# Kernel tuning notes

Hardware: AMD Instinct MI355X
Metric: run time of the kernel (lower is better)

## Reference

```python
import jax, jax.numpy as jnp
import numpy as np

TAU = 2.0      # LIF membrane time constant
ALPHA = 4.0    # spikingjelly surrogate.Sigmoid default alpha
V_TH = 1.0     # LIF threshold
EPS = 1e-5     # BatchNorm eps
NUM_HEADS = 8
TOPK = 64      # int(0.25 * 256)


@jax.custom_vjp
def spike_fn(x):
    # Heaviside spike with sigmoid surrogate gradient
    return (x >= 0.0).astype(x.dtype)

def _spike_fwd(x):
    return spike_fn(x), x

def _spike_bwd(x, g):
    s = jax.nn.sigmoid(ALPHA * x)
    return (g * ALPHA * s * (1.0 - s),)

spike_fn.defvjp(_spike_fwd, _spike_bwd)


def lif(x_seq):
    # Multi-step LIF (decay_input=True, hard reset to 0, detach_reset=True).
    # x_seq: [T, ...]; returns spikes of same shape.
    def step(v, x):
        v = v + (x - v) / TAU
        s = spike_fn(v - V_TH)
        v = v * (1.0 - jax.lax.stop_gradient(s))
        return v, s
    _, spikes = jax.lax.scan(step, jnp.zeros_like(x_seq[0]), x_seq)
    return spikes


def bn_eval(x, p):
    # BatchNorm in eval mode over last axis; p rows = [gamma, beta, mean, var]
    gamma, beta, mean, var = p[0], p[1], p[2], p[3]
    return (x - mean) * (gamma * jax.lax.rsqrt(var + EPS)) + beta


def setup_inputs() -> dict:
    key = jax.random.key(0)
    ks = jax.random.split(key, 10)
    T, B, N, C, H = 4, 16, 256, 256, NUM_HEADS
    w_scale = C ** -0.5
    return {
        "x": jax.random.normal(ks[0], (T, B, N, C), jnp.float32),
        "wq": jax.random.normal(ks[1], (C, C), jnp.float32) * w_scale,
        "wk": jax.random.normal(ks[2], (C, C), jnp.float32) * w_scale,
        "wv": jax.random.normal(ks[3], (C, C), jnp.float32) * w_scale,
        "bnq": jax.random.uniform(ks[4], (4, C), jnp.float32, 0.1, 1.0),
        "bnk": jax.random.uniform(ks[5], (4, C), jnp.float32, 0.1, 1.0),
        "bnv": jax.random.uniform(ks[6], (4, C), jnp.float32, 0.1, 1.0),
        "proj_w": jax.random.normal(ks[7], (C, C), jnp.float32) * w_scale,
        "proj_bn": jax.random.uniform(ks[8], (4, C), jnp.float32, 0.1, 1.0),
        "rel_bias_table": jax.random.normal(ks[9], (2 * N - 1, H), jnp.float32),
    }


def reference(x, wq, wk, wv, bnq, bnk, bnv, proj_w, proj_bn, rel_bias_table):
    T, B, N, C = x.shape
    H = NUM_HEADS
    D = C // H
    scale = C ** -0.5

    def qkv_branch(w, bn_p):
        h = jnp.einsum('tbnc,oc->tbno', x, w)   # Linear (no bias)
        h = bn_eval(h, bn_p)                    # eval BN is per-channel affine
        s = lif(h)                              # [T,B,N,C] spikes
        return s.reshape(T, B, N, H, D).transpose(0, 1, 3, 2, 4)  # [T,B,H,N,D]

    q = qkv_branch(wq, bnq)
    k = qkv_branch(wk, bnk)
    v = qkv_branch(wv, bnv)

    attn = jnp.einsum('tbhnd,tbhmd->tbhnm', q, k) * scale  # [T,B,H,N,N]

    # relative position bias gather: table[(j - i) + (N-1)] -> [N,N,H]
    rel_idx = (jnp.arange(N)[None, :] - jnp.arange(N)[:, None]) + (N - 1)
    rel_bias = rel_bias_table[rel_idx]                      # [N,N,H]
    attn = attn + rel_bias.transpose(2, 0, 1)[None, None]   # bcast over T,B

    # top-k keep per row, others zeroed (no softmax)
    kth = jax.lax.stop_gradient(jax.lax.top_k(attn, TOPK)[0][..., -1:])
    attn = jnp.where(attn >= kth, attn, 0.0)

    out = jnp.einsum('tbhnm,tbhmd->tbhnd', attn, v)
    out = out.transpose(0, 1, 3, 2, 4).reshape(T, B, N, C)
    out = lif(out)  # attn_lif

    # proj SpikLinearLayer: Linear -> BN(eval) -> LIF
    h = jnp.einsum('tbnc,oc->tbno', out, proj_w)
    h = bn_eval(h, proj_bn)
    return lif(h)
```

## Files before the change

### kernel.cpp

```cpp
#include <hip/hip_runtime.h>

typedef unsigned int u32;
typedef unsigned long long u64;

#define T_ 4
#define B_ 16
#define N_ 256
#define C_ 256
#define H_ 8
#define D_ 32
#define BNC_ 1048576
#define NELEM 4194304

__global__ __launch_bounds__(256) void gemm_bn(
    const float* __restrict__ A, const float* __restrict__ W,
    const float* __restrict__ bnp, float* __restrict__ Out)
{
  __shared__ float As[32][68];
  __shared__ float Ws[32][68];
  const int tid = threadIdx.x;
  const int m0 = blockIdx.y << 6;
  const int n0 = blockIdx.x << 6;
  const int tx = tid & 15, ty = tid >> 4;
  const int lrow = tid >> 3;
  const int lk = (tid & 7) << 2;

  float acc[4][4] = {};

  for (int k0 = 0; k0 < 256; k0 += 32) {
    float4 a0 = *(const float4*)(A + (size_t)(m0 + lrow) * 256 + k0 + lk);
    float4 a1 = *(const float4*)(A + (size_t)(m0 + lrow + 32) * 256 + k0 + lk);
    float4 w0 = *(const float4*)(W + (size_t)(n0 + lrow) * 256 + k0 + lk);
    float4 w1 = *(const float4*)(W + (size_t)(n0 + lrow + 32) * 256 + k0 + lk);
    __syncthreads();
    As[lk+0][lrow] = a0.x; As[lk+1][lrow] = a0.y; As[lk+2][lrow] = a0.z; As[lk+3][lrow] = a0.w;
    As[lk+0][lrow+32] = a1.x; As[lk+1][lrow+32] = a1.y; As[lk+2][lrow+32] = a1.z; As[lk+3][lrow+32] = a1.w;
    Ws[lk+0][lrow] = w0.x; Ws[lk+1][lrow] = w0.y; Ws[lk+2][lrow] = w0.z; Ws[lk+3][lrow] = w0.w;
    Ws[lk+0][lrow+32] = w1.x; Ws[lk+1][lrow+32] = w1.y; Ws[lk+2][lrow+32] = w1.z; Ws[lk+3][lrow+32] = w1.w;
    __syncthreads();
#pragma unroll
    for (int kk = 0; kk < 32; ++kk) {
      float4 av = *(const float4*)&As[kk][ty << 2];
      float4 bv = *(const float4*)&Ws[kk][tx << 2];
      acc[0][0] = fmaf(av.x, bv.x, acc[0][0]);
      acc[0][1] = fmaf(av.x, bv.y, acc[0][1]);
      acc[0][2] = fmaf(av.x, bv.z, acc[0][2]);
      acc[0][3] = fmaf(av.x, bv.w, acc[0][3]);
      acc[1][0] = fmaf(av.y, bv.x, acc[1][0]);
      acc[1][1] = fmaf(av.y, bv.y, acc[1][1]);
      acc[1][2] = fmaf(av.y, bv.z, acc[1][2]);
      acc[1][3] = fmaf(av.y, bv.w, acc[1][3]);
      acc[2][0] = fmaf(av.z, bv.x, acc[2][0]);
      acc[2][1] = fmaf(av.z, bv.y, acc[2][1]);
      acc[2][2] = fmaf(av.z, bv.z, acc[2][2]);
      acc[2][3] = fmaf(av.z, bv.w, acc[2][3]);
      acc[3][0] = fmaf(av.w, bv.x, acc[3][0]);
      acc[3][1] = fmaf(av.w, bv.y, acc[3][1]);
      acc[3][2] = fmaf(av.w, bv.z, acc[3][2]);
      acc[3][3] = fmaf(av.w, bv.w, acc[3][3]);
    }
  }

  const float* gma = bnp;
  const float* bta = bnp + 256;
  const float* mea = bnp + 512;
  const float* vra = bnp + 768;
  float sc[4], me[4], be[4];
#pragma unroll
  for (int jj = 0; jj < 4; ++jj) {
    int o = n0 + (tx << 2) + jj;
    sc[jj] = __fmul_rn(gma[o], 1.0f / sqrtf(__fadd_rn(vra[o], 1e-5f)));
    me[jj] = mea[o];
    be[jj] = bta[o];
  }
#pragma unroll
  for (int ii = 0; ii < 4; ++ii) {
    int row = m0 + (ty << 2) + ii;
    float4 y;
    y.x = __fadd_rn(__fmul_rn(__fsub_rn(acc[ii][0], me[0]), sc[0]), be[0]);
    y.y = __fadd_rn(__fmul_rn(__fsub_rn(acc[ii][1], me[1]), sc[1]), be[1]);
    y.z = __fadd_rn(__fmul_rn(__fsub_rn(acc[ii][2], me[2]), sc[2]), be[2]);
    y.w = __fadd_rn(__fmul_rn(__fsub_rn(acc[ii][3], me[3]), sc[3]), be[3]);
    *(float4*)(Out + (size_t)row * 256 + n0 + (tx << 2)) = y;
  }
}

__global__ __launch_bounds__(256) void lif_pack3(
    const float* __restrict__ h0, const float* __restrict__ h1,
    const float* __restrict__ h2,
    u32* __restrict__ m0p, u32* __restrict__ m1p, u32* __restrict__ m2p)
{
  const float* h = (blockIdx.y == 0) ? h0 : (blockIdx.y == 1) ? h1 : h2;
  u32* mask      = (blockIdx.y == 0) ? m0p : (blockIdx.y == 1) ? m1p : m2p;
  const int blk = blockIdx.x;
  const int b = blk >> 8, n = blk & 255;
  const int c = threadIdx.x;
  const int wave = c >> 6, lane = c & 63;
  const size_t idx = ((size_t)b * 256 + n) * 256 + c;
  float v = 0.0f;
#pragma unroll
  for (int t = 0; t < 4; ++t) {
    float xv = h[idx + (size_t)t * BNC_];
    v = __fadd_rn(v, __fmul_rn(__fsub_rn(xv, v), 0.5f));
    bool s = (v >= 1.0f);
    u64 bal = __ballot(s);
    const int h0i = wave << 1;
    u32* mptr = mask + ((size_t)(t * 16 + b) * 8) * 256 + n;
    if (lane == 0)  mptr[(size_t)h0i * 256]       = (u32)bal;
    if (lane == 32) mptr[(size_t)(h0i + 1) * 256] = (u32)(bal >> 32);
    v = s ? 0.0f : v;
  }
}

__global__ __launch_bounds__(256) void attn_topk_pv(
    const u32* __restrict__ qmask, const u32* __restrict__ kmask,
    const u32* __restrict__ vmask, const float* __restrict__ table,
    float* __restrict__ outPV)
{
  __shared__ __align__(16) u32 kms[256];
  __shared__ __align__(16) u32 vms[256];
  __shared__ __align__(16) float bias[511];
  __shared__ __align__(16) float arow[4][256];

  const int tbh = blockIdx.x;
  const int rg = blockIdx.y;
  const int hh = tbh & 7;
  const int tid = threadIdx.x;

  kms[tid] = kmask[((size_t)tbh << 8) + tid];
  vms[tid] = vmask[((size_t)tbh << 8) + tid];
  bias[tid] = table[tid * 8 + hh];
  if (tid < 255) bias[256 + tid] = table[(256 + tid) * 8 + hh];
  __syncthreads();

  const int wave = tid >> 6, lane = tid & 63;
  const int d = lane & 31, half = lane >> 5;

#pragma unroll
  for (int it = 0; it < 8; ++it) {
    const int i = (rg << 5) + (it << 2) + wave;
    const u32 qm = qmask[((size_t)tbh << 8) + i];
    float a[4];
    u32 u[4];
#pragma unroll
    for (int r = 0; r < 4; ++r) {
      const int j = lane + (r << 6);
      const int m = __popc(qm & kms[j]);
      float av = __fmul_rn((float)m, 0.0625f);
      av = __fadd_rn(av, bias[j - i + 255]);
      a[r] = av;
      const u32 bb = __float_as_uint(av);
      u[r] = bb ^ ((u32)((int)bb >> 31) | 0x80000000u);
    }
    u32 t = 0u;
#pragma unroll
    for (int bit = 31; bit >= 0; --bit) {
      const u32 cand = t | (1u << bit);
      const int cnt = __popcll(__ballot(u[0] >= cand)) +
                      __popcll(__ballot(u[1] >= cand)) +
                      __popcll(__ballot(u[2] >= cand)) +
                      __popcll(__ballot(u[3] >= cand));
      if (cnt >= 64) t = cand;
    }
#pragma unroll
    for (int r = 0; r < 4; ++r)
      arow[wave][lane + (r << 6)] = (u[r] >= t) ? a[r] : 0.0f;
    asm volatile("s_waitcnt lgkmcnt(0)" ::: "memory");

    float s = 0.0f;
#pragma unroll 8
    for (int jj = 0; jj < 32; ++jj) {
      const int j = (half << 7) + (jj << 2);
      float4 a4 = *(const float4*)&arow[wave][j];
      uint4 v4 = *(const uint4*)&vms[j];
      if ((v4.x >> d) & 1u) s += a4.x;
      if ((v4.y >> d) & 1u) s += a4.y;
      if ((v4.z >> d) & 1u) s += a4.z;
      if ((v4.w >> d) & 1u) s += a4.w;
    }
    s += __shfl_xor(s, 32, 64);
    if (half == 0)
      outPV[(((size_t)tbh << 8) + i) * 32 + d] = s;
  }
}

__global__ __launch_bounds__(256) void attn_lif(
    const float* __restrict__ pv, float* __restrict__ sout)
{
  const int blk = blockIdx.x;
  const int b = blk >> 8, n = blk & 255;
  const int c = threadIdx.x;
  const int hh = c >> 5, d = c & 31;
  float v = 0.0f;
#pragma unroll
  for (int t = 0; t < 4; ++t) {
    float xv = pv[(((size_t)(t * 16 + b) * 8 + hh) << 13) + (n << 5) + d];
    v = __fadd_rn(v, __fmul_rn(__fsub_rn(xv, v), 0.5f));
    bool s = (v >= 1.0f);
    sout[(((size_t)(t * 16 + b) << 8) + n) * 256 + c] = s ? 1.0f : 0.0f;
    v = s ? 0.0f : v;
  }
}

__global__ __launch_bounds__(256) void final_lif(
    const float* __restrict__ hp, float* __restrict__ out)
{
  const size_t base = (size_t)blockIdx.x * 256 + threadIdx.x;
  float v = 0.0f;
#pragma unroll
  for (int t = 0; t < 4; ++t) {
    float xv = hp[base + (size_t)t * BNC_];
    v = __fadd_rn(v, __fmul_rn(__fsub_rn(xv, v), 0.5f));
    bool s = (v >= 1.0f);
    out[base + (size_t)t * BNC_] = s ? 1.0f : 0.0f;
    v = s ? 0.0f : v;
  }
}

extern "C" void kernel_launch(void* const* d_in, const int* in_sizes, int n_in,
                              void* d_out, int out_size, void* d_ws, size_t ws_size,
                              hipStream_t stream) {
  const float* x       = (const float*)d_in[0];
  const float* wq      = (const float*)d_in[1];
  const float* wk      = (const float*)d_in[2];
  const float* wv      = (const float*)d_in[3];
  const float* bnq     = (const float*)d_in[4];
  const float* bnk     = (const float*)d_in[5];
  const float* bnv     = (const float*)d_in[6];
  const float* proj_w  = (const float*)d_in[7];
  const float* proj_bn = (const float*)d_in[8];
  const float* rtable  = (const float*)d_in[9];
  float* out = (float*)d_out;

  float* ws = (float*)d_ws;
  float* hq = ws;
  float* hk = ws + (size_t)NELEM;
  float* hv = ws + (size_t)NELEM * 2;
  u32* mq = (u32*)(ws + (size_t)NELEM * 3);
  u32* mk = mq + 131072;
  u32* mv = mk + 131072;
  float* outPV = hq;
  float* sout  = hk;
  float* hproj = hv;

  dim3 ggrid(4, 256);
  gemm_bn<<<ggrid, 256, 0, stream>>>(x, wq, bnq, hq);
  gemm_bn<<<ggrid, 256, 0, stream>>>(x, wk, bnk, hk);
  gemm_bn<<<ggrid, 256, 0, stream>>>(x, wv, bnv, hv);

  lif_pack3<<<dim3(4096, 3), 256, 0, stream>>>(hq, hk, hv, mq, mk, mv);

  attn_topk_pv<<<dim3(512, 8), 256, 0, stream>>>(mq, mk, mv, rtable, outPV);

  attn_lif<<<4096, 256, 0, stream>>>(outPV, sout);

  gemm_bn<<<ggrid, 256, 0, stream>>>(sout, proj_w, proj_bn, hproj);

  final_lif<<<4096, 256, 0, stream>>>(hproj, out);
}
```

Before: 378.7 us.

## Enlarge GEMM register tiles with prefetch and compact top-k entries for PV

```diff
diff --git a/kernel.cpp b/kernel.cpp
--- a/kernel.cpp
+++ b/kernel.cpp
@@ -12,76 +12,92 @@
 #define BNC_ 1048576
 #define NELEM 4194304
 
-__global__ __launch_bounds__(256) void gemm_bn(
+__global__ __launch_bounds__(128) void gemm_bn(
     const float* __restrict__ A, const float* __restrict__ W,
     const float* __restrict__ bnp, float* __restrict__ Out)
 {
-  __shared__ float As[32][68];
+  __shared__ float As[32][132];
   __shared__ float Ws[32][68];
   const int tid = threadIdx.x;
-  const int m0 = blockIdx.y << 6;
+  const int m0 = blockIdx.y << 7;
   const int n0 = blockIdx.x << 6;
-  const int tx = tid & 15, ty = tid >> 4;
-  const int lrow = tid >> 3;
-  const int lk = (tid & 7) << 2;
-
-  float acc[4][4] = {};
-
-  for (int k0 = 0; k0 < 256; k0 += 32) {
-    float4 a0 = *(const float4*)(A + (size_t)(m0 + lrow) * 256 + k0 + lk);
-    float4 a1 = *(const float4*)(A + (size_t)(m0 + lrow + 32) * 256 + k0 + lk);
-    float4 w0 = *(const float4*)(W + (size_t)(n0 + lrow) * 256 + k0 + lk);
-    float4 w1 = *(const float4*)(W + (size_t)(n0 + lrow + 32) * 256 + k0 + lk);
+  const int tx = tid & 7;
+  const int ty = tid >> 3;
+
+  float acc[8][8] = {};
+  float4 pa[8], pb[4];
+
+#define LOADA(k0)                                                          \
+  _Pragma("unroll") for (int c = 0; c < 8; ++c) {                          \
+    int id2 = tid + (c << 7); int row = id2 >> 3; int k4 = (id2 & 7) << 2; \
+    pa[c] = *(const float4*)(A + (size_t)(m0 + row) * 256 + (k0) + k4);    \
+  }
+#define LOADB(k0)                                                          \
+  _Pragma("unroll") for (int c = 0; c < 4; ++c) {                          \
+    int id2 = tid + (c << 7); int row = id2 >> 3; int k4 = (id2 & 7) << 2; \
+    pb[c] = *(const float4*)(W + (size_t)(n0 + row) * 256 + (k0) + k4);    \
+  }
+
+  LOADA(0); LOADB(0);
+
+  for (int s = 0; s < 8; ++s) {
+#pragma unroll
+    for (int c = 0; c < 8; ++c) {
+      int id2 = tid + (c << 7); int row = id2 >> 3; int k4 = (id2 & 7) << 2;
+      As[k4+0][row] = pa[c].x; As[k4+1][row] = pa[c].y;
+      As[k4+2][row] = pa[c].z; As[k4+3][row] = pa[c].w;
+    }
+#pragma unroll
+    for (int c = 0; c < 4; ++c) {
+      int id2 = tid + (c << 7); int row = id2 >> 3; int k4 = (id2 & 7) << 2;
+      Ws[k4+0][row] = pb[c].x; Ws[k4+1][row] = pb[c].y;
+      Ws[k4+2][row] = pb[c].z; Ws[k4+3][row] = pb[c].w;
+    }
     __syncthreads();
-    As[lk+0][lrow] = a0.x; As[lk+1][lrow] = a0.y; As[lk+2][lrow] = a0.z; As[lk+3][lrow] = a0.w;
-    As[lk+0][lrow+32] = a1.x; As[lk+1][lrow+32] = a1.y; As[lk+2][lrow+32] = a1.z; As[lk+3][lrow+32] = a1.w;
-    Ws[lk+0][lrow] = w0.x; Ws[lk+1][lrow] = w0.y; Ws[lk+2][lrow] = w0.z; Ws[lk+3][lrow] = w0.w;
-    Ws[lk+0][lrow+32] = w1.x; Ws[lk+1][lrow+32] = w1.y; Ws[lk+2][lrow+32] = w1.z; Ws[lk+3][lrow+32] = w1.w;
+    if (s < 7) { int k0n = (s + 1) << 5; LOADA(k0n); LOADB(k0n); }
+#pragma unroll
+    for (int kk = 0; kk < 32; ++kk) {
+      float4 a0 = *(const float4*)&As[kk][ty << 3];
+      float4 a1 = *(const float4*)&As[kk][(ty << 3) + 4];
+      float4 b0 = *(const float4*)&Ws[kk][tx << 3];
+      float4 b1 = *(const float4*)&Ws[kk][(tx << 3) + 4];
+      float av[8] = {a0.x,a0.y,a0.z,a0.w,a1.x,a1.y,a1.z,a1.w};
+      float bv[8] = {b0.x,b0.y,b0.z,b0.w,b1.x,b1.y,b1.z,b1.w};
+#pragma unroll
+      for (int ii = 0; ii < 8; ++ii)
+#pragma unroll
+        for (int jj = 0; jj < 8; ++jj)
+          acc[ii][jj] = fmaf(av[ii], bv[jj], acc[ii][jj]);
+    }
     __syncthreads();
-#pragma unroll
-    for (int kk = 0; kk < 32; ++kk) {
-      float4 av = *(const float4*)&As[kk][ty << 2];
-      float4 bv = *(const float4*)&Ws[kk][tx << 2];
-      acc[0][0] = fmaf(av.x, bv.x, acc[0][0]);
-      acc[0][1] = fmaf(av.x, bv.y, acc[0][1]);
-      acc[0][2] = fmaf(av.x, bv.z, acc[0][2]);
-      acc[0][3] = fmaf(av.x, bv.w, acc[0][3]);
-      acc[1][0] = fmaf(av.y, bv.x, acc[1][0]);
-      acc[1][1] = fmaf(av.y, bv.y, acc[1][1]);
-      acc[1][2] = fmaf(av.y, bv.z, acc[1][2]);
-      acc[1][3] = fmaf(av.y, bv.w, acc[1][3]);
-      acc[2][0] = fmaf(av.z, bv.x, acc[2][0]);
-      acc[2][1] = fmaf(av.z, bv.y, acc[2][1]);
-      acc[2][2] = fmaf(av.z, bv.z, acc[2][2]);
-      acc[2][3] = fmaf(av.z, bv.w, acc[2][3]);
-      acc[3][0] = fmaf(av.w, bv.x, acc[3][0]);
-      acc[3][1] = fmaf(av.w, bv.y, acc[3][1]);
-      acc[3][2] = fmaf(av.w, bv.z, acc[3][2]);
-      acc[3][3] = fmaf(av.w, bv.w, acc[3][3]);
-    }
   }
 
   const float* gma = bnp;
   const float* bta = bnp + 256;
   const float* mea = bnp + 512;
   const float* vra = bnp + 768;
-  float sc[4], me[4], be[4];
-#pragma unroll
-  for (int jj = 0; jj < 4; ++jj) {
-    int o = n0 + (tx << 2) + jj;
+  float sc[8], me[8], be[8];
+#pragma unroll
+  for (int jj = 0; jj < 8; ++jj) {
+    int o = n0 + (tx << 3) + jj;
     sc[jj] = __fmul_rn(gma[o], 1.0f / sqrtf(__fadd_rn(vra[o], 1e-5f)));
     me[jj] = mea[o];
     be[jj] = bta[o];
   }
 #pragma unroll
-  for (int ii = 0; ii < 4; ++ii) {
-    int row = m0 + (ty << 2) + ii;
-    float4 y;
-    y.x = __fadd_rn(__fmul_rn(__fsub_rn(acc[ii][0], me[0]), sc[0]), be[0]);
-    y.y = __fadd_rn(__fmul_rn(__fsub_rn(acc[ii][1], me[1]), sc[1]), be[1]);
-    y.z = __fadd_rn(__fmul_rn(__fsub_rn(acc[ii][2], me[2]), sc[2]), be[2]);
-    y.w = __fadd_rn(__fmul_rn(__fsub_rn(acc[ii][3], me[3]), sc[3]), be[3]);
-    *(float4*)(Out + (size_t)row * 256 + n0 + (tx << 2)) = y;
+  for (int ii = 0; ii < 8; ++ii) {
+    int row = m0 + (ty << 3) + ii;
+    float4 y0, y1;
+    y0.x = __fadd_rn(__fmul_rn(__fsub_rn(acc[ii][0], me[0]), sc[0]), be[0]);
+    y0.y = __fadd_rn(__fmul_rn(__fsub_rn(acc[ii][1], me[1]), sc[1]), be[1]);
+    y0.z = __fadd_rn(__fmul_rn(__fsub_rn(acc[ii][2], me[2]), sc[2]), be[2]);
+    y0.w = __fadd_rn(__fmul_rn(__fsub_rn(acc[ii][3], me[3]), sc[3]), be[3]);
+    y1.x = __fadd_rn(__fmul_rn(__fsub_rn(acc[ii][4], me[4]), sc[4]), be[4]);
+    y1.y = __fadd_rn(__fmul_rn(__fsub_rn(acc[ii][5], me[5]), sc[5]), be[5]);
+    y1.z = __fadd_rn(__fmul_rn(__fsub_rn(acc[ii][6], me[6]), sc[6]), be[6]);
+    y1.w = __fadd_rn(__fmul_rn(__fsub_rn(acc[ii][7], me[7]), sc[7]), be[7]);
+    *(float4*)(Out + (size_t)row * 256 + n0 + (tx << 3))     = y0;
+    *(float4*)(Out + (size_t)row * 256 + n0 + (tx << 3) + 4) = y1;
   }
 }
 
@@ -117,18 +133,14 @@
     const u32* __restrict__ vmask, const float* __restrict__ table,
     float* __restrict__ outPV)
 {
-  __shared__ __align__(16) u32 kms[256];
-  __shared__ __align__(16) u32 vms[256];
   __shared__ __align__(16) float bias[511];
-  __shared__ __align__(16) float arow[4][256];
+  __shared__ __align__(16) u64 comp[4][2][132];
 
   const int tbh = blockIdx.x;
   const int rg = blockIdx.y;
   const int hh = tbh & 7;
   const int tid = threadIdx.x;
 
-  kms[tid] = kmask[((size_t)tbh << 8) + tid];
-  vms[tid] = vmask[((size_t)tbh << 8) + tid];
   bias[tid] = table[tid * 8 + hh];
   if (tid < 255) bias[256 + tid] = table[(256 + tid) * 8 + hh];
   __syncthreads();
@@ -136,16 +148,25 @@
   const int wave = tid >> 6, lane = tid & 63;
   const int d = lane & 31, half = lane >> 5;
 
-#pragma unroll
+  u32 kmr[4], vmr[4];
+#pragma unroll
+  for (int r = 0; r < 4; ++r) {
+    kmr[r] = kmask[((size_t)tbh << 8) + lane + (r << 6)];
+    vmr[r] = vmask[((size_t)tbh << 8) + lane + (r << 6)];
+  }
+  const u64 below = (1ull << lane) - 1ull;
+  u64* const clo = &comp[wave][0][0];
+  u64* const chi = &comp[wave][1][0];
+
+#pragma unroll 1
   for (int it = 0; it < 8; ++it) {
     const int i = (rg << 5) + (it << 2) + wave;
     const u32 qm = qmask[((size_t)tbh << 8) + i];
-    float a[4];
-    u32 u[4];
+    float a[4]; u32 u[4];
 #pragma unroll
     for (int r = 0; r < 4; ++r) {
       const int j = lane + (r << 6);
-      const int m = __popc(qm & kms[j]);
+      const int m = __popc(qm & kmr[r]);
       float av = __fmul_rn((float)m, 0.0625f);
       av = __fadd_rn(av, bias[j - i + 255]);
       a[r] = av;
@@ -153,30 +174,41 @@
       u[r] = bb ^ ((u32)((int)bb >> 31) | 0x80000000u);
     }
     u32 t = 0u;
-#pragma unroll
     for (int bit = 31; bit >= 0; --bit) {
       const u32 cand = t | (1u << bit);
       const int cnt = __popcll(__ballot(u[0] >= cand)) +
                       __popcll(__ballot(u[1] >= cand)) +
                       __popcll(__ballot(u[2] >= cand)) +
                       __popcll(__ballot(u[3] >= cand));
-      if (cnt >= 64) t = cand;
-    }
-#pragma unroll
-    for (int r = 0; r < 4; ++r)
-      arow[wave][lane + (r << 6)] = (u[r] >= t) ? a[r] : 0.0f;
+      if (cnt >= 64) { t = cand; if (cnt == 64) break; }
+    }
+    const u64 B0 = __ballot(u[0] >= t), B1 = __ballot(u[1] >= t);
+    const u64 B2 = __ballot(u[2] >= t), B3 = __ballot(u[3] >= t);
+    const int c0 = __popcll(B0), c1 = __popcll(B1);
+    const int c2 = __popcll(B2), c3 = __popcll(B3);
+    const int p0 = __popcll(B0 & below);
+    const int p1 = c0 + __popcll(B1 & below);
+    const int p2 = __popcll(B2 & below);
+    const int p3 = c2 + __popcll(B3 & below);
+    if (u[0] >= t) clo[p0] = ((u64)vmr[0] << 32) | (u64)__float_as_uint(a[0]);
+    if (u[1] >= t) clo[p1] = ((u64)vmr[1] << 32) | (u64)__float_as_uint(a[1]);
+    if (u[2] >= t) chi[p2] = ((u64)vmr[2] << 32) | (u64)__float_as_uint(a[2]);
+    if (u[3] >= t) chi[p3] = ((u64)vmr[3] << 32) | (u64)__float_as_uint(a[3]);
+    const int nlo = c0 + c1, nhi = c2 + c3;
+    if (lane < 2)      clo[nlo + lane] = 0ull;
+    else if (lane < 4) chi[nhi + lane - 2] = 0ull;
     asm volatile("s_waitcnt lgkmcnt(0)" ::: "memory");
 
+    const int n = half ? nhi : nlo;
+    const u64* cp = half ? chi : clo;
+    const int gn = (n + 1) >> 1;
     float s = 0.0f;
-#pragma unroll 8
-    for (int jj = 0; jj < 32; ++jj) {
-      const int j = (half << 7) + (jj << 2);
-      float4 a4 = *(const float4*)&arow[wave][j];
-      uint4 v4 = *(const uint4*)&vms[j];
-      if ((v4.x >> d) & 1u) s += a4.x;
-      if ((v4.y >> d) & 1u) s += a4.y;
-      if ((v4.z >> d) & 1u) s += a4.z;
-      if ((v4.w >> d) & 1u) s += a4.w;
+    for (int g = 0; g < gn; ++g) {
+      uint4 e = *(const uint4*)(cp + ((size_t)g << 1));
+      const u32 mk0 = (u32)__builtin_amdgcn_sbfe((int)e.y, d, 1);
+      s = __fadd_rn(s, __uint_as_float(e.x & mk0));
+      const u32 mk1 = (u32)__builtin_amdgcn_sbfe((int)e.w, d, 1);
+      s = __fadd_rn(s, __uint_as_float(e.z & mk1));
     }
     s += __shfl_xor(s, 32, 64);
     if (half == 0)
@@ -243,10 +275,10 @@
   float* sout  = hk;
   float* hproj = hv;
 
-  dim3 ggrid(4, 256);
-  gemm_bn<<<ggrid, 256, 0, stream>>>(x, wq, bnq, hq);
-  gemm_bn<<<ggrid, 256, 0, stream>>>(x, wk, bnk, hk);
-  gemm_bn<<<ggrid, 256, 0, stream>>>(x, wv, bnv, hv);
+  dim3 ggrid(4, 128);
+  gemm_bn<<<ggrid, 128, 0, stream>>>(x, wq, bnq, hq);
+  gemm_bn<<<ggrid, 128, 0, stream>>>(x, wk, bnk, hk);
+  gemm_bn<<<ggrid, 128, 0, stream>>>(x, wv, bnv, hv);
 
   lif_pack3<<<dim3(4096, 3), 256, 0, stream>>>(hq, hk, hv, mq, mk, mv);
 
@@ -254,7 +286,7 @@
 
   attn_lif<<<4096, 256, 0, stream>>>(outPV, sout);
 
-  gemm_bn<<<ggrid, 256, 0, stream>>>(sout, proj_w, proj_bn, hproj);
+  gemm_bn<<<ggrid, 128, 0, stream>>>(sout, proj_w, proj_bn, hproj);
 
   final_lif<<<4096, 256, 0, stream>>>(hproj, out);
 }
```

After: 335.3 us. 1.13x faster.
